# Optimization experiments

Measured on AMD Instinct MI355X. Metric: run time of the kernel, lower is better.

The kernel has to match this reference:

```python
import jax, jax.numpy as jnp
import numpy as np

K = 3          # kernel size
STRIDE = 1
PAD = 1
DIL = 1


def setup_inputs() -> dict:
    key = jax.random.key(0)
    k1, k2, k3 = jax.random.split(key, 3)
    N, Cin, H, W = 8, 128, 64, 64
    Cout = 128
    x = jax.random.normal(k1, (N, Cin, H, W), dtype=jnp.float32)
    # offset channels: 2 * deformable_groups * K*K = 18, interleaved (dy, dx) per tap
    offset = jax.random.normal(k2, (N, 2 * K * K, H, W), dtype=jnp.float32)
    weight = jax.random.normal(k3, (Cout, Cin, K, K), dtype=jnp.float32) / np.sqrt(Cin * K * K)
    return {"x": x, "offset": offset, "weight": weight}


def _deform_conv(x, offset, weight):
    N, Cin, H, W = x.shape
    Cout = weight.shape[0]
    KK = K * K
    Ho, Wo = offset.shape[2], offset.shape[3]

    off = offset.reshape(N, KK, 2, Ho, Wo)
    dy = off[:, :, 0]  # [N, KK, Ho, Wo]
    dx = off[:, :, 1]

    kh = jnp.repeat(jnp.arange(K), K).astype(x.dtype)   # [KK]
    kw = jnp.tile(jnp.arange(K), K).astype(x.dtype)     # [KK]
    base_i = (jnp.arange(Ho) * STRIDE - PAD).astype(x.dtype)  # [Ho]
    base_j = (jnp.arange(Wo) * STRIDE - PAD).astype(x.dtype)  # [Wo]

    # Sampling positions: [N, KK, Ho, Wo]
    py = base_i[None, None, :, None] + (kh * DIL)[None, :, None, None] + dy
    px = base_j[None, None, None, :] + (kw * DIL)[None, :, None, None] + dx

    y0 = jnp.floor(py)
    x0 = jnp.floor(px)
    wy1 = py - y0
    wx1 = px - x0
    wy0 = 1.0 - wy1
    wx0 = 1.0 - wx1
    y0i = y0.astype(jnp.int32)
    x0i = x0.astype(jnp.int32)
    y1i = y0i + 1
    x1i = x0i + 1

    x_flat = x.reshape(N, Cin, H * W)

    def gather(yi, xi):
        # zero-padding outside the image
        mask = ((yi >= 0) & (yi < H) & (xi >= 0) & (xi < W)).astype(x.dtype)
        idx = jnp.clip(yi, 0, H - 1) * W + jnp.clip(xi, 0, W - 1)  # [N,KK,Ho,Wo]
        v = jnp.take_along_axis(x_flat, idx.reshape(N, 1, -1), axis=2)  # [N,Cin,KK*Ho*Wo]
        v = v.reshape(N, Cin, KK, Ho, Wo)
        return v * mask[:, None]

    sampled = (gather(y0i, x0i) * (wy0 * wx0)[:, None]
               + gather(y0i, x1i) * (wy0 * wx1)[:, None]
               + gather(y1i, x0i) * (wy1 * wx0)[:, None]
               + gather(y1i, x1i) * (wy1 * wx1)[:, None])  # [N,Cin,KK,Ho,Wo]

    w = weight.reshape(Cout, Cin, KK)
    return jnp.einsum('nckij,ock->noij', sampled, w)


def reference(x, offset, weight):
    return _deform_conv(x, offset, weight)
```

## Files before the change

kernel.cpp:

```cpp
#include <hip/hip_runtime.h>


#define H  64
#define W  64
#define CIN 128
#define COUT 128
#define NB 8
#define KK 9
#define SROW (CIN + 8)

typedef short bf16x8 __attribute__((ext_vector_type(8)));
typedef float f32x4  __attribute__((ext_vector_type(4)));

__device__ __forceinline__ unsigned short f2bf(float f) {
    unsigned u = __builtin_bit_cast(unsigned, f);
    u += 0x7FFFu + ((u >> 16) & 1u);
    return (unsigned short)(u >> 16);
}
__device__ __forceinline__ unsigned cvt_pk_bf16(float lo, float hi) {
    unsigned r;
    asm("v_cvt_pk_bf16_f32 %0, %1, %2" : "=v"(r) : "v"(lo), "v"(hi));
    return r;
}
__device__ __forceinline__ float lo_f(unsigned u) { return __builtin_bit_cast(float, u << 16); }
__device__ __forceinline__ float hi_f(unsigned u) { return __builtin_bit_cast(float, u & 0xFFFF0000u); }

__global__ void prep_all(const float* __restrict__ x, const float* __restrict__ w,
                         unsigned short* __restrict__ xt, unsigned short* __restrict__ wt) {
    int b = blockIdx.x;
    int t = threadIdx.x;
    if (b >= NB * H) {
        int idx = (b - NB * H) * 256 + t;
        if (idx < KK * COUT * CIN) {
            int kk = idx / (COUT * CIN);
            int r  = idx - kk * (COUT * CIN);
            int co = r >> 7;
            int c  = r & 127;
            wt[idx] = f2bf(w[(co * CIN + c) * KK + kk]);
        }
        return;
    }
    __shared__ float tile[CIN][W + 4];
    int n = b & 7, y = b >> 3;
    const float* src = x + ((size_t)n * CIN * H + y) * W;
    #pragma unroll
    for (int it = 0; it < 8; ++it) {
        int idx = it * 256 + t;
        int c  = idx >> 4;
        int x4 = (idx & 15) << 2;
        int xs = (x4 + ((c >> 5) << 4)) & 63;
        *(float4*)&tile[c][xs] = *(const float4*)(src + (size_t)c * H * W + x4);
    }
    __syncthreads();
    int xp = t >> 2;
    int cbch = (t & 3) << 5;
    int xr = (xp + ((cbch >> 5) << 4)) & 63;
    unsigned short* dst = xt + (((size_t)(n * H + y) * W + xp) * CIN + cbch);
    unsigned rr[16];
    #pragma unroll
    for (int i = 0; i < 16; ++i)
        rr[i] = cvt_pk_bf16(tile[cbch + 2 * i][xr], tile[cbch + 2 * i + 1][xr]);
    #pragma unroll
    for (int i = 0; i < 4; ++i)
        ((uint4*)dst)[i] = make_uint4(rr[4*i], rr[4*i+1], rr[4*i+2], rr[4*i+3]);
}

struct GatherCtx {
    const unsigned short *c00, *c01, *c10, *c11;
    float w00, w01, w10, w11;
};

__device__ __forceinline__ GatherCtx gather_setup(float dy, float dx, int ho, int wo, int kk,
                                                  const unsigned short* xbase) {
    GatherCtx g;
    float py = (float)(ho - 1 + kk / 3) + dy;
    float px = (float)(wo - 1 + kk % 3) + dx;
    float y0f = floorf(py), x0f = floorf(px);
    float wy1 = py - y0f, wx1 = px - x0f;
    float wy0 = 1.f - wy1, wx0 = 1.f - wx1;
    int y0 = (int)y0f, x0 = (int)x0f;
    int y1 = y0 + 1, x1 = x0 + 1;
    bool vy0 = (unsigned)y0 < (unsigned)H, vy1 = (unsigned)y1 < (unsigned)H;
    bool vx0 = (unsigned)x0 < (unsigned)W, vx1 = (unsigned)x1 < (unsigned)W;
    g.w00 = (vy0 && vx0) ? wy0 * wx0 : 0.f;
    g.w01 = (vy0 && vx1) ? wy0 * wx1 : 0.f;
    g.w10 = (vy1 && vx0) ? wy1 * wx0 : 0.f;
    g.w11 = (vy1 && vx1) ? wy1 * wx1 : 0.f;
    int yc0 = min(max(y0, 0), H - 1), yc1 = min(max(y1, 0), H - 1);
    int xc0 = min(max(x0, 0), W - 1), xc1 = min(max(x1, 0), W - 1);
    const unsigned short* r0 = xbase + (size_t)yc0 * W * CIN;
    const unsigned short* r1 = xbase + (size_t)yc1 * W * CIN;
    g.c00 = r0 + xc0 * CIN;  g.c01 = r0 + xc1 * CIN;
    g.c10 = r1 + xc0 * CIN;  g.c11 = r1 + xc1 * CIN;
    return g;
}

__device__ __forceinline__ void gather_issue(const GatherCtx& g, uint4* gv) {
    #pragma unroll
    for (int j = 0; j < 4; ++j) {
        gv[4*j+0] = *(const uint4*)(g.c00 + 8*j);
        gv[4*j+1] = *(const uint4*)(g.c01 + 8*j);
        gv[4*j+2] = *(const uint4*)(g.c10 + 8*j);
        gv[4*j+3] = *(const uint4*)(g.c11 + 8*j);
    }
}

__device__ __forceinline__ void gather_blend_store(const GatherCtx& g, const uint4* gv,
                                                   unsigned short* dst) {
    #pragma unroll
    for (int j = 0; j < 4; ++j) {
        const unsigned* a0 = (const unsigned*)&gv[4*j+0];
        const unsigned* a1 = (const unsigned*)&gv[4*j+1];
        const unsigned* a2 = (const unsigned*)&gv[4*j+2];
        const unsigned* a3 = (const unsigned*)&gv[4*j+3];
        unsigned rr[4];
        #pragma unroll
        for (int i = 0; i < 4; ++i) {
            float v0 = g.w00*lo_f(a0[i]) + g.w01*lo_f(a1[i]) + g.w10*lo_f(a2[i]) + g.w11*lo_f(a3[i]);
            float v1 = g.w00*hi_f(a0[i]) + g.w01*hi_f(a1[i]) + g.w10*hi_f(a2[i]) + g.w11*hi_f(a3[i]);
            rr[i] = cvt_pk_bf16(v0, v1);
        }
        *(uint4*)(dst + 8*j) = make_uint4(rr[0], rr[1], rr[2], rr[3]);
    }
}

#define LOADB(dst, kkv) { \
    const unsigned short* wk_ = wlane + ((size_t)(kkv) << 14);  \
    _Pragma("unroll") \
    for (int nt_ = 0; nt_ < 2; ++nt_) \
        _Pragma("unroll") \
        for (int ct_ = 0; ct_ < 4; ++ct_) \
            dst[nt_][ct_] = *(const bf16x8*)(wk_ + (nt_ << 11) + (ct_ << 5)); }

#define MFMA_PHASE(PAR, BREG) { \
    _Pragma("unroll") \
    for (int ct_ = 0; ct_ < 4; ++ct_) { \
        bf16x8 a_[4]; \
        _Pragma("unroll") \
        for (int mt_ = 0; mt_ < 4; ++mt_) \
            a_[mt_] = *(const bf16x8*)&samp[PAR][lm + (mt_ << 4)][(ct_ << 5) + (lq << 3)]; \
        _Pragma("unroll") \
        for (int mt_ = 0; mt_ < 4; ++mt_) { \
            acc[mt_][0] = __builtin_amdgcn_mfma_f32_16x16x32_bf16(a_[mt_], BREG[0][ct_], acc[mt_][0], 0, 0, 0); \
            acc[mt_][1] = __builtin_amdgcn_mfma_f32_16x16x32_bf16(a_[mt_], BREG[1][ct_], acc[mt_][1], 0, 0, 0); } } }

#define ITER(kkv, PAR, BCUR, BNXT, LAST) { \
    GatherCtx g_; uint4 gv_[16]; \
    if (!(LAST)) { \
        g_ = gather_setup(dyA, dxA, ho, p, (kkv) + 1, xbase); \
        gather_issue(g_, gv_); \
        LOADB(BNXT, (kkv) + 1); \
        if ((kkv) < KK - 2) { \
            dyA = offbase[(size_t)(2 * ((kkv) + 2)) * H * W]; \
            dxA = offbase[(size_t)(2 * ((kkv) + 2) + 1) * H * W]; \
        } \
    } \
    __builtin_amdgcn_sched_barrier(0);  \
    MFMA_PHASE(PAR, BCUR); \
    if (!(LAST)) { \
        gather_blend_store(g_, gv_, &samp[1 - (PAR)][p][cb]); \
        __syncthreads(); \
    } }

__global__ __launch_bounds__(256, 2) void deform_main(
        const float* __restrict__ offs, const unsigned short* __restrict__ xt,
        const unsigned short* __restrict__ wt, float* __restrict__ out) {
    __shared__ __attribute__((aligned(16))) unsigned short samp[2][64][SROW];

    int b = blockIdx.x;
    int n = b & 7, ho = b >> 3;
    int t = threadIdx.x;
    int lane = t & 63, wv = t >> 6;
    int lm = lane & 15, lq = lane >> 4;
    int cobase = wv << 5;

    f32x4 acc[4][2];
    #pragma unroll
    for (int mt = 0; mt < 4; ++mt)
        #pragma unroll
        for (int nt = 0; nt < 2; ++nt) acc[mt][nt] = f32x4{0.f, 0.f, 0.f, 0.f};

    int p  = t >> 2;
    int cb = (t & 3) << 5;
    const float* offbase = offs + (size_t)n * 2 * KK * H * W + (size_t)ho * W + p;
    const unsigned short* xbase = xt + (size_t)n * H * W * CIN + cb;
    const unsigned short* wlane = wt + (((size_t)(cobase + lm)) << 7) + (lq << 3);

    bf16x8 bA[2][4], bB[2][4];

    float dyA = offbase[0];
    float dxA = offbase[(size_t)H * W];
    {
        GatherCtx g = gather_setup(dyA, dxA, ho, p, 0, xbase);
        uint4 gv[16];
        gather_issue(g, gv);
        LOADB(bA, 0);
        dyA = offbase[(size_t)2 * H * W];
        dxA = offbase[(size_t)3 * H * W];
        gather_blend_store(g, gv, &samp[0][p][cb]);
        __syncthreads();
    }

    for (int k2 = 0; k2 < 4; ++k2) {
        int kk = k2 << 1;
        ITER(kk,     0, bA, bB, false);
        ITER(kk + 1, 1, bB, bA, false);
    }
    ITER(8, 0, bA, bB, true);

    #pragma unroll
    for (int mt = 0; mt < 4; ++mt) {
        int wob = (mt << 4) + (lq << 2);
        #pragma unroll
        for (int nt = 0; nt < 2; ++nt) {
            int co = cobase + (nt << 4) + lm;
            *(f32x4*)(out + (((size_t)(n * COUT + co) * H + ho) * W + wob)) = acc[mt][nt];
        }
    }
}

extern "C" void kernel_launch(void* const* d_in, const int* in_sizes, int n_in,
                              void* d_out, int out_size, void* d_ws, size_t ws_size,
                              hipStream_t stream) {
    const float* x      = (const float*)d_in[0];
    const float* offset = (const float*)d_in[1];
    const float* weight = (const float*)d_in[2];
    float* out = (float*)d_out;

    unsigned short* xt = (unsigned short*)d_ws;
    unsigned short* wt = (unsigned short*)((char*)d_ws + (size_t)NB*H*W*CIN*2);

    int wblocks = (KK * COUT * CIN + 255) / 256;
    hipLaunchKernelGGL(prep_all, dim3(NB * H + wblocks), dim3(256), 0, stream,
                       x, weight, xt, wt);
    hipLaunchKernelGGL(deform_main, dim3(NB * H), dim3(256), 0, stream,
                       offset, xt, wt, out);
}
```

Baseline: 115.2 us.

## Split each output row across two blocks and raise occupancy to four blocks per CU

Each block now covers half an output row (32 pixels) instead of all 64, which doubles the grid and halves per-thread gather work, accumulators and LDS staging. Weight registers are single-buffered and reloaded after the MFMA phase, and MFMA runs at raised wave priority. Launch bounds move from two to four blocks per CU to hide gather latency with more waves. The cost is that every block now loads the full weight set, so weight traffic from global/L2 doubles, and the weight load is no longer overlapped with the MFMA phase.

```diff
diff --git a/kernel.cpp b/kernel.cpp
--- a/kernel.cpp
+++ b/kernel.cpp
@@ -97,7 +97,7 @@
 
 __device__ __forceinline__ void gather_issue(const GatherCtx& g, uint4* gv) {
     #pragma unroll
-    for (int j = 0; j < 4; ++j) {
+    for (int j = 0; j < 2; ++j) {
         gv[4*j+0] = *(const uint4*)(g.c00 + 8*j);
         gv[4*j+1] = *(const uint4*)(g.c01 + 8*j);
         gv[4*j+2] = *(const uint4*)(g.c10 + 8*j);
@@ -108,7 +108,7 @@
 __device__ __forceinline__ void gather_blend_store(const GatherCtx& g, const uint4* gv,
                                                    unsigned short* dst) {
     #pragma unroll
-    for (int j = 0; j < 4; ++j) {
+    for (int j = 0; j < 2; ++j) {
         const unsigned* a0 = (const unsigned*)&gv[4*j+0];
         const unsigned* a1 = (const unsigned*)&gv[4*j+1];
         const unsigned* a2 = (const unsigned*)&gv[4*j+2];
@@ -124,77 +124,81 @@
     }
 }
 
-#define LOADB(dst, kkv) { \
+#define LOADB(kkv) { \
     const unsigned short* wk_ = wlane + ((size_t)(kkv) << 14);  \
     _Pragma("unroll") \
     for (int nt_ = 0; nt_ < 2; ++nt_) \
         _Pragma("unroll") \
         for (int ct_ = 0; ct_ < 4; ++ct_) \
-            dst[nt_][ct_] = *(const bf16x8*)(wk_ + (nt_ << 11) + (ct_ << 5)); }
-
-#define MFMA_PHASE(PAR, BREG) { \
+            bW[nt_][ct_] = *(const bf16x8*)(wk_ + (nt_ << 11) + (ct_ << 5)); }
+
+#define MFMA_PHASE(PAR) { \
+    __builtin_amdgcn_s_setprio(1); \
     _Pragma("unroll") \
     for (int ct_ = 0; ct_ < 4; ++ct_) { \
-        bf16x8 a_[4]; \
+        bf16x8 a_[2]; \
         _Pragma("unroll") \
-        for (int mt_ = 0; mt_ < 4; ++mt_) \
+        for (int mt_ = 0; mt_ < 2; ++mt_) \
             a_[mt_] = *(const bf16x8*)&samp[PAR][lm + (mt_ << 4)][(ct_ << 5) + (lq << 3)]; \
         _Pragma("unroll") \
-        for (int mt_ = 0; mt_ < 4; ++mt_) { \
-            acc[mt_][0] = __builtin_amdgcn_mfma_f32_16x16x32_bf16(a_[mt_], BREG[0][ct_], acc[mt_][0], 0, 0, 0); \
-            acc[mt_][1] = __builtin_amdgcn_mfma_f32_16x16x32_bf16(a_[mt_], BREG[1][ct_], acc[mt_][1], 0, 0, 0); } } }
-
-#define ITER(kkv, PAR, BCUR, BNXT, LAST) { \
-    GatherCtx g_; uint4 gv_[16]; \
+        for (int mt_ = 0; mt_ < 2; ++mt_) { \
+            acc[mt_][0] = __builtin_amdgcn_mfma_f32_16x16x32_bf16(a_[mt_], bW[0][ct_], acc[mt_][0], 0, 0, 0); \
+            acc[mt_][1] = __builtin_amdgcn_mfma_f32_16x16x32_bf16(a_[mt_], bW[1][ct_], acc[mt_][1], 0, 0, 0); } } \
+    __builtin_amdgcn_s_setprio(0); }
+
+#define ITER(kkv, PAR, LAST) { \
+    GatherCtx g_; uint4 gv_[8]; \
     if (!(LAST)) { \
-        g_ = gather_setup(dyA, dxA, ho, p, (kkv) + 1, xbase); \
+        g_ = gather_setup(dyA, dxA, ho, wo_g, (kkv) + 1, xbase); \
         gather_issue(g_, gv_); \
-        LOADB(BNXT, (kkv) + 1); \
         if ((kkv) < KK - 2) { \
             dyA = offbase[(size_t)(2 * ((kkv) + 2)) * H * W]; \
             dxA = offbase[(size_t)(2 * ((kkv) + 2) + 1) * H * W]; \
         } \
     } \
     __builtin_amdgcn_sched_barrier(0);  \
-    MFMA_PHASE(PAR, BCUR); \
+    MFMA_PHASE(PAR); \
+    __builtin_amdgcn_sched_barrier(0);  \
     if (!(LAST)) { \
+        LOADB((kkv) + 1); \
         gather_blend_store(g_, gv_, &samp[1 - (PAR)][p][cb]); \
         __syncthreads(); \
     } }
 
-__global__ __launch_bounds__(256, 2) void deform_main(
+__global__ __launch_bounds__(256, 4) void deform_main(
         const float* __restrict__ offs, const unsigned short* __restrict__ xt,
         const unsigned short* __restrict__ wt, float* __restrict__ out) {
-    __shared__ __attribute__((aligned(16))) unsigned short samp[2][64][SROW];
+    __shared__ __attribute__((aligned(16))) unsigned short samp[2][32][SROW];
 
     int b = blockIdx.x;
-    int n = b & 7, ho = b >> 3;
+    int n = b & 7, ho = (b >> 3) & 63, hf = b >> 9;
     int t = threadIdx.x;
     int lane = t & 63, wv = t >> 6;
     int lm = lane & 15, lq = lane >> 4;
     int cobase = wv << 5;
 
-    f32x4 acc[4][2];
-    #pragma unroll
-    for (int mt = 0; mt < 4; ++mt)
+    f32x4 acc[2][2];
+    #pragma unroll
+    for (int mt = 0; mt < 2; ++mt)
         #pragma unroll
         for (int nt = 0; nt < 2; ++nt) acc[mt][nt] = f32x4{0.f, 0.f, 0.f, 0.f};
 
-    int p  = t >> 2;
-    int cb = (t & 3) << 5;
-    const float* offbase = offs + (size_t)n * 2 * KK * H * W + (size_t)ho * W + p;
+    int p  = t >> 3;
+    int cb = (t & 7) << 4;
+    int wo_g = (hf << 5) + p;
+    const float* offbase = offs + (size_t)n * 2 * KK * H * W + (size_t)ho * W + wo_g;
     const unsigned short* xbase = xt + (size_t)n * H * W * CIN + cb;
     const unsigned short* wlane = wt + (((size_t)(cobase + lm)) << 7) + (lq << 3);
 
-    bf16x8 bA[2][4], bB[2][4];
+    bf16x8 bW[2][4];
 
     float dyA = offbase[0];
     float dxA = offbase[(size_t)H * W];
     {
-        GatherCtx g = gather_setup(dyA, dxA, ho, p, 0, xbase);
-        uint4 gv[16];
+        GatherCtx g = gather_setup(dyA, dxA, ho, wo_g, 0, xbase);
+        uint4 gv[8];
         gather_issue(g, gv);
-        LOADB(bA, 0);
+        LOADB(0);
         dyA = offbase[(size_t)2 * H * W];
         dxA = offbase[(size_t)3 * H * W];
         gather_blend_store(g, gv, &samp[0][p][cb]);
@@ -202,15 +206,14 @@
     }
 
     for (int k2 = 0; k2 < 4; ++k2) {
-        int kk = k2 << 1;
-        ITER(kk,     0, bA, bB, false);
-        ITER(kk + 1, 1, bB, bA, false);
-    }
-    ITER(8, 0, bA, bB, true);
-
-    #pragma unroll
-    for (int mt = 0; mt < 4; ++mt) {
-        int wob = (mt << 4) + (lq << 2);
+        ITER(2 * k2,     0, false);
+        ITER(2 * k2 + 1, 1, false);
+    }
+    ITER(8, 0, true);
+
+    #pragma unroll
+    for (int mt = 0; mt < 2; ++mt) {
+        int wob = (hf << 5) + (mt << 4) + (lq << 2);
         #pragma unroll
         for (int nt = 0; nt < 2; ++nt) {
             int co = cobase + (nt << 4) + lm;
@@ -233,6 +236,6 @@
     int wblocks = (KK * COUT * CIN + 255) / 256;
     hipLaunchKernelGGL(prep_all, dim3(NB * H + wblocks), dim3(256), 0, stream,
                        x, weight, xt, wt);
-    hipLaunchKernelGGL(deform_main, dim3(NB * H), dim3(256), 0, stream,
+    hipLaunchKernelGGL(deform_main, dim3(NB * H * 2), dim3(256), 0, stream,
                        offset, xt, wt, out);
 }
```

Measured after the change: 120.6 us. +4.7%, slower.

## Split deform conv into producer gather warps and consumer MFMA warps

Applied to the files above, without the earlier changes.

The main kernel now launches 512 threads. Four producer waves do the bilinear gather into the double-buffered shared tile, and four consumer waves run the MFMA accumulation, synchronising once per tap. The weight prep kernel writes weights in a layout pre-swizzled to match each lane's fragment, so consumers load B operands with contiguous per-lane 16-byte reads, and compute runs at raised priority. This trades the in-warp software pipelining and register-prefetched B for warp specialisation. It risks lower occupancy from the launch bounds change, and the B loads are now issued just before use instead of one tap ahead.

```diff
diff --git a/kernel.cpp b/kernel.cpp
--- a/kernel.cpp
+++ b/kernel.cpp
@@ -32,11 +32,16 @@
     if (b >= NB * H) {
         int idx = (b - NB * H) * 256 + t;
         if (idx < KK * COUT * CIN) {
-            int kk = idx / (COUT * CIN);
-            int r  = idx - kk * (COUT * CIN);
-            int co = r >> 7;
-            int c  = r & 127;
-            wt[idx] = f2bf(w[(co * CIN + c) * KK + kk]);
+            int e  = idx & 7;
+            int lq = (idx >> 3) & 3;
+            int lm = (idx >> 5) & 15;
+            int ct = (idx >> 9) & 3;
+            int nt = (idx >> 11) & 1;
+            int c4 = (idx >> 12) & 3;
+            int kk = idx >> 14;
+            int co = (c4 << 5) + (nt << 4) + lm;
+            int ch = (ct << 5) + (lq << 3) + e;
+            wt[idx] = f2bf(w[(co * CIN + ch) * KK + kk]);
         }
         return;
     }
@@ -124,45 +129,7 @@
     }
 }
 
-#define LOADB(dst, kkv) { \
-    const unsigned short* wk_ = wlane + ((size_t)(kkv) << 14);  \
-    _Pragma("unroll") \
-    for (int nt_ = 0; nt_ < 2; ++nt_) \
-        _Pragma("unroll") \
-        for (int ct_ = 0; ct_ < 4; ++ct_) \
-            dst[nt_][ct_] = *(const bf16x8*)(wk_ + (nt_ << 11) + (ct_ << 5)); }
-
-#define MFMA_PHASE(PAR, BREG) { \
-    _Pragma("unroll") \
-    for (int ct_ = 0; ct_ < 4; ++ct_) { \
-        bf16x8 a_[4]; \
-        _Pragma("unroll") \
-        for (int mt_ = 0; mt_ < 4; ++mt_) \
-            a_[mt_] = *(const bf16x8*)&samp[PAR][lm + (mt_ << 4)][(ct_ << 5) + (lq << 3)]; \
-        _Pragma("unroll") \
-        for (int mt_ = 0; mt_ < 4; ++mt_) { \
-            acc[mt_][0] = __builtin_amdgcn_mfma_f32_16x16x32_bf16(a_[mt_], BREG[0][ct_], acc[mt_][0], 0, 0, 0); \
-            acc[mt_][1] = __builtin_amdgcn_mfma_f32_16x16x32_bf16(a_[mt_], BREG[1][ct_], acc[mt_][1], 0, 0, 0); } } }
-
-#define ITER(kkv, PAR, BCUR, BNXT, LAST) { \
-    GatherCtx g_; uint4 gv_[16]; \
-    if (!(LAST)) { \
-        g_ = gather_setup(dyA, dxA, ho, p, (kkv) + 1, xbase); \
-        gather_issue(g_, gv_); \
-        LOADB(BNXT, (kkv) + 1); \
-        if ((kkv) < KK - 2) { \
-            dyA = offbase[(size_t)(2 * ((kkv) + 2)) * H * W]; \
-            dxA = offbase[(size_t)(2 * ((kkv) + 2) + 1) * H * W]; \
-        } \
-    } \
-    __builtin_amdgcn_sched_barrier(0);  \
-    MFMA_PHASE(PAR, BCUR); \
-    if (!(LAST)) { \
-        gather_blend_store(g_, gv_, &samp[1 - (PAR)][p][cb]); \
-        __syncthreads(); \
-    } }
-
-__global__ __launch_bounds__(256, 2) void deform_main(
+__global__ __launch_bounds__(512, 4) void deform_main(
         const float* __restrict__ offs, const unsigned short* __restrict__ xt,
         const unsigned short* __restrict__ wt, float* __restrict__ out) {
     __shared__ __attribute__((aligned(16))) unsigned short samp[2][64][SROW];
@@ -171,8 +138,46 @@
     int n = b & 7, ho = b >> 3;
     int t = threadIdx.x;
     int lane = t & 63, wv = t >> 6;
+    bool producer = (wv >= 4);
+
+    if (producer) {
+        int t2 = t - 256;
+        int p  = t2 >> 2;
+        int cb = (t2 & 3) << 5;
+        const float* offbase = offs + (size_t)n * 2 * KK * H * W + (size_t)ho * W + p;
+        const unsigned short* xbase = xt + (size_t)n * H * W * CIN + cb;
+
+        float dyA = offbase[0];
+        float dxA = offbase[(size_t)H * W];
+        {
+            GatherCtx g = gather_setup(dyA, dxA, ho, p, 0, xbase);
+            uint4 gv[16];
+            gather_issue(g, gv);
+            dyA = offbase[(size_t)2 * H * W];
+            dxA = offbase[(size_t)3 * H * W];
+            gather_blend_store(g, gv, &samp[0][p][cb]);
+        }
+        __syncthreads();
+        for (int k = 0; k < KK; ++k) {
+            if (k < KK - 1) {
+                int tap = k + 1;
+                GatherCtx g = gather_setup(dyA, dxA, ho, p, tap, xbase);
+                uint4 gv[16];
+                gather_issue(g, gv);
+                if (k < KK - 2) {
+                    dyA = offbase[(size_t)(2 * (tap + 1)) * H * W];
+                    dxA = offbase[(size_t)(2 * (tap + 1) + 1) * H * W];
+                }
+                gather_blend_store(g, gv, &samp[tap & 1][p][cb]);
+            }
+            __syncthreads();
+        }
+        return;
+    }
+
     int lm = lane & 15, lq = lane >> 4;
     int cobase = wv << 5;
+    int slot = (lm << 2) + lq;
 
     f32x4 acc[4][2];
     #pragma unroll
@@ -180,33 +185,34 @@
         #pragma unroll
         for (int nt = 0; nt < 2; ++nt) acc[mt][nt] = f32x4{0.f, 0.f, 0.f, 0.f};
 
-    int p  = t >> 2;
-    int cb = (t & 3) << 5;
-    const float* offbase = offs + (size_t)n * 2 * KK * H * W + (size_t)ho * W + p;
-    const unsigned short* xbase = xt + (size_t)n * H * W * CIN + cb;
-    const unsigned short* wlane = wt + (((size_t)(cobase + lm)) << 7) + (lq << 3);
-
-    bf16x8 bA[2][4], bB[2][4];
-
-    float dyA = offbase[0];
-    float dxA = offbase[(size_t)H * W];
-    {
-        GatherCtx g = gather_setup(dyA, dxA, ho, p, 0, xbase);
-        uint4 gv[16];
-        gather_issue(g, gv);
-        LOADB(bA, 0);
-        dyA = offbase[(size_t)2 * H * W];
-        dxA = offbase[(size_t)3 * H * W];
-        gather_blend_store(g, gv, &samp[0][p][cb]);
+    const unsigned short* wvbase = wt + ((size_t)wv << 12) + (slot << 3);
+
+    __syncthreads();
+    for (int k = 0; k < KK; ++k) {
+        const unsigned short* wkb = wvbase + ((size_t)(k << 2) << 12);
+        bf16x8 bW[2][4];
+        #pragma unroll
+        for (int nt = 0; nt < 2; ++nt)
+            #pragma unroll
+            for (int ct = 0; ct < 4; ++ct)
+                bW[nt][ct] = *(const bf16x8*)(wkb + (((nt << 2) + ct) << 9));
+
+        __builtin_amdgcn_s_setprio(1);
+        #pragma unroll
+        for (int ct = 0; ct < 4; ++ct) {
+            bf16x8 a[4];
+            #pragma unroll
+            for (int mt = 0; mt < 4; ++mt)
+                a[mt] = *(const bf16x8*)&samp[k & 1][lm + (mt << 4)][(ct << 5) + (lq << 3)];
+            #pragma unroll
+            for (int mt = 0; mt < 4; ++mt) {
+                acc[mt][0] = __builtin_amdgcn_mfma_f32_16x16x32_bf16(a[mt], bW[0][ct], acc[mt][0], 0, 0, 0);
+                acc[mt][1] = __builtin_amdgcn_mfma_f32_16x16x32_bf16(a[mt], bW[1][ct], acc[mt][1], 0, 0, 0);
+            }
+        }
+        __builtin_amdgcn_s_setprio(0);
         __syncthreads();
     }
-
-    for (int k2 = 0; k2 < 4; ++k2) {
-        int kk = k2 << 1;
-        ITER(kk,     0, bA, bB, false);
-        ITER(kk + 1, 1, bB, bA, false);
-    }
-    ITER(8, 0, bA, bB, true);
 
     #pragma unroll
     for (int mt = 0; mt < 4; ++mt) {
@@ -233,6 +239,6 @@
     int wblocks = (KK * COUT * CIN + 255) / 256;
     hipLaunchKernelGGL(prep_all, dim3(NB * H + wblocks), dim3(256), 0, stream,
                        x, weight, xt, wt);
-    hipLaunchKernelGGL(deform_main, dim3(NB * H), dim3(256), 0, stream,
+    hipLaunchKernelGGL(deform_main, dim3(NB * H), dim3(512), 0, stream,
                        offset, xt, wt, out);
 }
```

After: 111.0 us. -3.6%, faster.
